# Performance work log

Hardware: AMD Instinct MI355X
Metric: run time of the kernel (lower is better)

Reference implementation:

```python
import jax, jax.numpy as jnp
import numpy as np

BS, SL, D_IN, D_MODEL, H = 4, 128, 512, 512, 8
DP = D_MODEL // H


def setup_inputs() -> dict:
    key = jax.random.key(0)
    ks = jax.random.split(key, 12)
    s = 0.02
    inp = {
        "q": jax.random.normal(ks[0], (BS, SL, D_IN), jnp.float32),
        "k": jax.random.normal(ks[1], (BS, SL, D_IN), jnp.float32),
        "v": jax.random.normal(ks[2], (BS, SL, D_IN), jnp.float32),
    }
    j = jnp.arange(SL)
    # mask[t, jk] = 1.0 for the zero-padded slots jk > t in the shuffled sequence for step t
    mask2d = (j[None, :] > j[:, None]).astype(jnp.float32)  # (SL, SL)
    inp["mask"] = mask2d[None, :, None, None, :]            # (1, SL, 1, 1, SL)
    for i, n in enumerate(["wq", "wk", "wv", "dense"]):
        din = D_IN if n != "dense" else D_MODEL
        inp[n + "_w"] = jax.random.normal(ks[3 + 2 * i], (din, D_MODEL), jnp.float32) * s
        inp[n + "_b"] = jnp.zeros((D_MODEL,), jnp.float32)
    return inp


def _shuffle_idx(key, sl):
    # Row t of returned idx: random permutation of [0..t-1], then t, then t+1.. (padding slots).
    u = jax.random.uniform(key, (sl, sl))
    j = jnp.arange(sl)
    t = j[:, None]
    sort_keys = jnp.where(j[None, :] < t, u, j[None, :].astype(jnp.float32) + 2.0)
    return jnp.argsort(sort_keys, axis=-1)  # (sl, sl) int32


def _split_heads_shuffled(x, idx, valid):
    # x: (bs, sl, d) -> (bs, sl, H, sl, DP); padding slots (j > t) zeroed like torch plc_holder
    bs, sl, d = x.shape
    xt = x[:, idx, :] * valid[None, :, :, None]  # (bs, sl, sl, d)
    xt = xt.reshape(bs, sl, sl, H, DP)
    return xt.transpose(0, 1, 3, 2, 4)


def reference(q, k, v, mask, wq_w, wq_b, wk_w, wk_b, wv_w, wv_b, dense_w, dense_b):
    bs, sl, _ = q.shape
    j = jnp.arange(sl)
    valid = (j[None, :] <= j[:, None]).astype(q.dtype)  # (sl, sl)
    pkey = jax.random.key(42)
    idx_q = _shuffle_idx(jax.random.fold_in(pkey, 0), sl)
    idx_k = _shuffle_idx(jax.random.fold_in(pkey, 1), sl)
    idx_v = _shuffle_idx(jax.random.fold_in(pkey, 2), sl)

    qp = q @ wq_w + wq_b
    kp = k @ wk_w + wk_b
    vp = v @ wv_w + wv_b

    qh = _split_heads_shuffled(qp, idx_q, valid)  # (bs, sl, H, sl, DP)
    kh = _split_heads_shuffled(kp, idx_k, valid)
    vh = _split_heads_shuffled(vp, idx_v, valid)

    logits = jnp.einsum('bthqd,bthkd->bthqk', qh, kh) / jnp.sqrt(jnp.float32(DP))
    logits = logits + mask * (-1e9)
    attn = jax.nn.softmax(logits, axis=-1)          # (bs, sl, H, sl, sl)
    ctx = jnp.einsum('bthqk,bthkd->bthqd', attn, vh)  # (bs, sl, H, sl, DP)

    ctx = ctx.transpose(0, 1, 3, 2, 4).reshape(bs, sl, sl, H * DP)
    eff = ctx[:, j, j, :]                           # query row t of step t (the token itself)
    out = eff @ dense_w + dense_b                   # (bs, sl, d_model); dropout p=0 -> identity
    return (out, attn)
```

## Files before the change

### kernel.cpp

```cpp
#include <hip/hip_runtime.h>
#include <stdint.h>


#define BSZ 4
#define SLEN 128
#define DMODEL 512
#define NHEAD 8
#define HDIM 64

__device__ __forceinline__ uint32_t rotl32(uint32_t v, int d) {
  return (v << d) | (v >> (32 - d));
}

__device__ __forceinline__ void tf2x32(uint32_t k0, uint32_t k1, uint32_t x0,
                                       uint32_t x1, uint32_t& y0, uint32_t& y1) {
  uint32_t ks2 = k0 ^ k1 ^ 0x1BD11BDAu;
  x0 += k0; x1 += k1;
#define TF_R(r) { x0 += x1; x1 = rotl32(x1, (r)); x1 ^= x0; }
  TF_R(13) TF_R(15) TF_R(26) TF_R(6)
  x0 += k1;  x1 += ks2 + 1u;
  TF_R(17) TF_R(29) TF_R(16) TF_R(24)
  x0 += ks2; x1 += k0 + 2u;
  TF_R(13) TF_R(15) TF_R(26) TF_R(6)
  x0 += k0;  x1 += k1 + 3u;
  TF_R(17) TF_R(29) TF_R(16) TF_R(24)
  x0 += k1;  x1 += ks2 + 4u;
  TF_R(13) TF_R(15) TF_R(26) TF_R(6)
  x0 += ks2; x1 += k0 + 5u;
#undef TF_R
  y0 = x0; y1 = x1;
}

__global__ __launch_bounds__(128) void idx_kernel(int* __restrict__ idx) {
  const int m = blockIdx.x;
  const int t = blockIdx.y;
  const int j = threadIdx.x;
  __shared__ float u[SLEN];
  uint32_t fk0, fk1;
  tf2x32(0u, 42u, 0u, (uint32_t)m, fk0, fk1);
  const int flat = t * SLEN + j;
  uint32_t y0, y1;
  tf2x32(fk0, fk1, 0u, (uint32_t)flat, y0, y1);
  uint32_t bits = y0 ^ y1;
  float uu = __uint_as_float((bits >> 9) | 0x3f800000u) - 1.0f;
  u[j] = uu;
  __syncthreads();
  int* row = idx + (m * SLEN + t) * SLEN;
  if (j >= t) {
    row[j] = j;
  } else {
    int rank = 0;
    for (int i = 0; i < t; ++i) {
      float ui = u[i];
      rank += ((ui < uu) || (ui == uu && i < j)) ? 1 : 0;
    }
    row[rank] = j;
  }
}

__device__ __forceinline__ void gemm512_body(const float* __restrict__ A,
                                             const float* __restrict__ W,
                                             const float* __restrict__ bias,
                                             float* __restrict__ C,
                                             float* As , float* Ws ) {
  const int tid = threadIdx.x;
  const int tx = tid & 15, ty = tid >> 4;
  const int row0 = blockIdx.y * 64, col0 = blockIdx.x * 64;
  const int lr = tid >> 2, lc = (tid & 3) << 2;
  const int wr = tid >> 4, wc = (tid & 15) << 2;
  float acc[4][4] = {};
  for (int k0 = 0; k0 < 512; k0 += 16) {
    float4 av = *(const float4*)(A + (size_t)(row0 + lr) * 512 + k0 + lc);
    float4 wv = *(const float4*)(W + (size_t)(k0 + wr) * 512 + col0 + wc);
    As[lr * 17 + lc + 0] = av.x; As[lr * 17 + lc + 1] = av.y;
    As[lr * 17 + lc + 2] = av.z; As[lr * 17 + lc + 3] = av.w;
    *(float4*)(Ws + wr * 64 + wc) = wv;
    __syncthreads();
#pragma unroll
    for (int kk = 0; kk < 16; ++kk) {
      float a[4], b[4];
#pragma unroll
      for (int i = 0; i < 4; ++i) a[i] = As[(ty * 4 + i) * 17 + kk];
#pragma unroll
      for (int jj = 0; jj < 4; ++jj) b[jj] = Ws[kk * 64 + tx * 4 + jj];
#pragma unroll
      for (int i = 0; i < 4; ++i)
#pragma unroll
        for (int jj = 0; jj < 4; ++jj) acc[i][jj] += a[i] * b[jj];
    }
    __syncthreads();
  }
#pragma unroll
  for (int i = 0; i < 4; ++i) {
    int r = row0 + ty * 4 + i, c = col0 + tx * 4;
    float4 o;
    o.x = acc[i][0] + bias[c + 0];
    o.y = acc[i][1] + bias[c + 1];
    o.z = acc[i][2] + bias[c + 2];
    o.w = acc[i][3] + bias[c + 3];
    *(float4*)(C + (size_t)r * 512 + c) = o;
  }
}

__global__ __launch_bounds__(256) void proj_kernel(
    const float* __restrict__ q, const float* __restrict__ k, const float* __restrict__ v,
    const float* __restrict__ wq, const float* __restrict__ wk, const float* __restrict__ wv,
    const float* __restrict__ bq, const float* __restrict__ bk, const float* __restrict__ bv,
    float* __restrict__ qp, float* __restrict__ kp, float* __restrict__ vp) {
  __shared__ float As[64 * 17];
  __shared__ float Ws[16 * 64];
  const float* A; const float* W; const float* B; float* C;
  if (blockIdx.z == 0)      { A = q; W = wq; B = bq; C = qp; }
  else if (blockIdx.z == 1) { A = k; W = wk; B = bk; C = kp; }
  else                      { A = v; W = wv; B = bv; C = vp; }
  gemm512_body(A, W, B, C, As, Ws);
}

__global__ __launch_bounds__(256) void dense_kernel(const float* __restrict__ A,
                                                    const float* __restrict__ W,
                                                    const float* __restrict__ B,
                                                    float* __restrict__ C) {
  __shared__ float As[64 * 17];
  __shared__ float Ws[16 * 64];
  gemm512_body(A, W, B, C, As, Ws);
}

__global__ __launch_bounds__(256) void s_kernel(const float* __restrict__ qp,
                                                const float* __restrict__ kp,
                                                float* __restrict__ S) {
  const int h = blockIdx.x, b = blockIdx.y;
  const int tid = threadIdx.x;
  __shared__ float qs[SLEN * 33];
  __shared__ float ks[SLEN * 33];
  const float* qbase = qp + ((size_t)b * SLEN) * DMODEL + h * HDIM;
  const float* kbase = kp + ((size_t)b * SLEN) * DMODEL + h * HDIM;
  const int i0 = (tid >> 4) * 8, j0 = (tid & 15) * 8;
  float acc[8][8] = {};
  for (int d0 = 0; d0 < HDIM; d0 += 32) {
    __syncthreads();
    for (int it = 0; it < 4; ++it) {
      int flat = it * 256 + tid;
      int row = flat >> 3;
      int c4 = (flat & 7) << 2;
      float4 a = *(const float4*)(qbase + (size_t)row * DMODEL + d0 + c4);
      float4 bb = *(const float4*)(kbase + (size_t)row * DMODEL + d0 + c4);
      qs[row * 33 + c4 + 0] = a.x;  qs[row * 33 + c4 + 1] = a.y;
      qs[row * 33 + c4 + 2] = a.z;  qs[row * 33 + c4 + 3] = a.w;
      ks[row * 33 + c4 + 0] = bb.x; ks[row * 33 + c4 + 1] = bb.y;
      ks[row * 33 + c4 + 2] = bb.z; ks[row * 33 + c4 + 3] = bb.w;
    }
    __syncthreads();
    for (int d = 0; d < 32; ++d) {
      float a[8], bb[8];
#pragma unroll
      for (int r = 0; r < 8; ++r) a[r] = qs[(i0 + r) * 33 + d];
#pragma unroll
      for (int c = 0; c < 8; ++c) bb[c] = ks[(j0 + c) * 33 + d];
#pragma unroll
      for (int r = 0; r < 8; ++r)
#pragma unroll
        for (int c = 0; c < 8; ++c) acc[r][c] += a[r] * bb[c];
    }
  }
  float* Sb = S + (size_t)(b * NHEAD + h) * SLEN * SLEN;
#pragma unroll
  for (int r = 0; r < 8; ++r) {
    float4 o0, o1;
    o0.x = acc[r][0] * 0.125f; o0.y = acc[r][1] * 0.125f;
    o0.z = acc[r][2] * 0.125f; o0.w = acc[r][3] * 0.125f;
    o1.x = acc[r][4] * 0.125f; o1.y = acc[r][5] * 0.125f;
    o1.z = acc[r][6] * 0.125f; o1.w = acc[r][7] * 0.125f;
    *(float4*)(Sb + (size_t)(i0 + r) * SLEN + j0) = o0;
    *(float4*)(Sb + (size_t)(i0 + r) * SLEN + j0 + 4) = o1;
  }
}

__global__ __launch_bounds__(128) void ef_kernel(const float* __restrict__ S,
                                                 float* __restrict__ E,
                                                 float* __restrict__ Ft) {
  const int bh = blockIdx.x;
  const int i = threadIdx.x;
  __shared__ float m127s[SLEN];
  const float* Sb = S + (size_t)bh * SLEN * SLEN;
  const float* Srow = Sb + (size_t)i * SLEN;
  float m = -3.402823466e38f;
  for (int j = 0; j < SLEN; ++j) m = fmaxf(m, Srow[j]);
  m127s[i] = m;
  float rm = -3.402823466e38f, rl = 0.f;
  float* Fb = Ft + (size_t)bh * SLEN * SLEN;
  for (int t = 0; t < SLEN; ++t) {
    float sv = Srow[t];
    float nm = fmaxf(rm, sv);
    rl = rl * __expf(rm - nm) + __expf(sv - nm);
    rm = nm;
    Fb[t * SLEN + i] = __expf(m - nm) / rl;
  }
  __syncthreads();
  float* Eb = E + (size_t)bh * SLEN * SLEN;
  for (int flat = i; flat < SLEN * SLEN; flat += SLEN) {
    int r = flat >> 7;
    Eb[flat] = __expf(Sb[flat] - m127s[r]);
  }
}

__global__ __launch_bounds__(256) void attn_kernel(const float* __restrict__ E,
                                                   const float* __restrict__ Ft,
                                                   const int* __restrict__ idx,
                                                   const float* __restrict__ vp,
                                                   float* __restrict__ attn_out,
                                                   float* __restrict__ eff) {
  const int h = blockIdx.x, t = blockIdx.y, b = blockIdx.z;
  const int tid = threadIdx.x;
  const int wave = tid >> 6, lane = tid & 63;
  __shared__ int iqs[SLEN], iks[SLEN], ivs[SLEN];
  __shared__ float arow[SLEN];
  if (tid < SLEN) {
    iqs[tid] = idx[(0 * SLEN + t) * SLEN + tid];
    iks[tid] = idx[(1 * SLEN + t) * SLEN + tid];
    ivs[tid] = idx[(2 * SLEN + t) * SLEN + tid];
  }
  __syncthreads();
  const int bh = b * NHEAD + h;
  const float* Eb = E + (size_t)bh * SLEN * SLEN;
  const float* Fb = Ft + ((size_t)bh * SLEN + t) * SLEN;
  const float inv = 1.0f / (float)(t + 1);
  float* obase = attn_out + ((size_t)((b * SLEN + t) * NHEAD + h)) * SLEN * SLEN;
  const int k0 = lane * 2, k1 = lane * 2 + 1;
  for (int q = wave; q < SLEN; q += 4) {
    float2 val;
    if (q <= t) {
      int iq = iqs[q];
      float f = Fb[iq];
      const float* Er = Eb + (size_t)iq * SLEN;
      val.x = (k0 <= t) ? Er[iks[k0]] * f : 0.f;
      val.y = (k1 <= t) ? Er[iks[k1]] * f : 0.f;
    } else {
      val.x = (k0 <= t) ? inv : 0.f;
      val.y = (k1 <= t) ? inv : 0.f;
    }
    *(float2*)(obase + (size_t)q * SLEN + k0) = val;
    if (q == t) { arow[k0] = val.x; arow[k1] = val.y; }
  }
  __syncthreads();
  if (tid < HDIM) {
    const int d = tid;
    const float* vb = vp + (size_t)b * SLEN * DMODEL + h * HDIM + d;
    float acc = 0.f;
    for (int k = 0; k <= t; ++k) acc += arow[k] * vb[(size_t)ivs[k] * DMODEL];
    eff[((size_t)b * SLEN + t) * DMODEL + h * HDIM + d] = acc;
  }
}

extern "C" void kernel_launch(void* const* d_in, const int* in_sizes, int n_in,
                              void* d_out, int out_size, void* d_ws, size_t ws_size,
                              hipStream_t stream) {
  const float* q    = (const float*)d_in[0];
  const float* k    = (const float*)d_in[1];
  const float* v    = (const float*)d_in[2];
  const float* wq_w = (const float*)d_in[4];
  const float* wq_b = (const float*)d_in[5];
  const float* wk_w = (const float*)d_in[6];
  const float* wk_b = (const float*)d_in[7];
  const float* wv_w = (const float*)d_in[8];
  const float* wv_b = (const float*)d_in[9];
  const float* dw   = (const float*)d_in[10];
  const float* db   = (const float*)d_in[11];

  float* out  = (float*)d_out;
  float* attn = out + 262144;

  int*   idx = (int*)d_ws;
  float* wsf = (float*)d_ws;
  float* qp  = wsf + 49152;
  float* kp  = qp + 262144;
  float* vp  = kp + 262144;
  float* S   = vp + 262144;
  float* E   = S + 524288;
  float* Ft  = E + 524288;
  float* eff = Ft + 524288;
  (void)in_sizes; (void)n_in; (void)out_size; (void)ws_size;

  idx_kernel<<<dim3(3, 128, 1), 128, 0, stream>>>(idx);
  proj_kernel<<<dim3(8, 8, 3), 256, 0, stream>>>(q, k, v, wq_w, wk_w, wv_w,
                                                 wq_b, wk_b, wv_b, qp, kp, vp);
  s_kernel<<<dim3(8, 4, 1), 256, 0, stream>>>(qp, kp, S);
  ef_kernel<<<dim3(32, 1, 1), 128, 0, stream>>>(S, E, Ft);
  attn_kernel<<<dim3(8, 128, 4), 256, 0, stream>>>(E, Ft, idx, vp, attn, eff);
  dense_kernel<<<dim3(8, 8, 1), 256, 0, stream>>>(eff, dw, db, out);
}
```

Before: 439.6 us.

## Fuse score, exp and prefix-normalizer kernels; store E as bf16

Merges the S and E/F kernels into one. The max, exp and running-sum normalizers are computed from the register tile using shared-memory reductions, and the serial per-row scan in a 32-block kernel goes away. E is stored in bf16, which halves its traffic in the attention gather but adds rounding error to the attn output. The attention kernel also caches the F row in LDS, hoists the key indices, and splits the context reduction across all four waves. The prefix normalizer is now computed from exps relative to the global row max rather than the running-max rescaling form, which may change numerics.

```diff
diff --git a/kernel.cpp b/kernel.cpp
--- a/kernel.cpp
+++ b/kernel.cpp
@@ -29,6 +29,14 @@
   x0 += ks2; x1 += k0 + 5u;
 #undef TF_R
   y0 = x0; y1 = x1;
+}
+
+__device__ __forceinline__ uint16_t f32_to_bf16(float v) {
+  uint32_t x = __float_as_uint(v);
+  return (uint16_t)((x + 0x7FFFu + ((x >> 16) & 1u)) >> 16);
+}
+__device__ __forceinline__ float bf16_to_f32(uint16_t b) {
+  return __uint_as_float(((uint32_t)b) << 16);
 }
 
 __global__ __launch_bounds__(128) void idx_kernel(int* __restrict__ idx) {
@@ -125,16 +133,20 @@
   gemm512_body(A, W, B, C, As, Ws);
 }
 
-__global__ __launch_bounds__(256) void s_kernel(const float* __restrict__ qp,
-                                                const float* __restrict__ kp,
-                                                float* __restrict__ S) {
+__global__ __launch_bounds__(256) void sef_kernel(const float* __restrict__ qp,
+                                                  const float* __restrict__ kp,
+                                                  uint16_t* __restrict__ E,
+                                                  float* __restrict__ Ft) {
   const int h = blockIdx.x, b = blockIdx.y;
   const int tid = threadIdx.x;
-  __shared__ float qs[SLEN * 33];
-  __shared__ float ks[SLEN * 33];
+  __shared__ float qs[32 * 132];
+  __shared__ float ks[32 * 132];
+  __shared__ float redm[128 * 16];
+  __shared__ float csum[128 * 16];
+  __shared__ float m127s[SLEN];
   const float* qbase = qp + ((size_t)b * SLEN) * DMODEL + h * HDIM;
   const float* kbase = kp + ((size_t)b * SLEN) * DMODEL + h * HDIM;
-  const int i0 = (tid >> 4) * 8, j0 = (tid & 15) * 8;
+  const int i0 = (tid >> 4) * 8, jg = tid & 15, j0 = jg * 8;
   float acc[8][8] = {};
   for (int d0 = 0; d0 < HDIM; d0 += 32) {
     __syncthreads();
@@ -144,66 +156,79 @@
       int c4 = (flat & 7) << 2;
       float4 a = *(const float4*)(qbase + (size_t)row * DMODEL + d0 + c4);
       float4 bb = *(const float4*)(kbase + (size_t)row * DMODEL + d0 + c4);
-      qs[row * 33 + c4 + 0] = a.x;  qs[row * 33 + c4 + 1] = a.y;
-      qs[row * 33 + c4 + 2] = a.z;  qs[row * 33 + c4 + 3] = a.w;
-      ks[row * 33 + c4 + 0] = bb.x; ks[row * 33 + c4 + 1] = bb.y;
-      ks[row * 33 + c4 + 2] = bb.z; ks[row * 33 + c4 + 3] = bb.w;
+      qs[(c4 + 0) * 132 + row] = a.x;  qs[(c4 + 1) * 132 + row] = a.y;
+      qs[(c4 + 2) * 132 + row] = a.z;  qs[(c4 + 3) * 132 + row] = a.w;
+      ks[(c4 + 0) * 132 + row] = bb.x; ks[(c4 + 1) * 132 + row] = bb.y;
+      ks[(c4 + 2) * 132 + row] = bb.z; ks[(c4 + 3) * 132 + row] = bb.w;
     }
     __syncthreads();
     for (int d = 0; d < 32; ++d) {
-      float a[8], bb[8];
-#pragma unroll
-      for (int r = 0; r < 8; ++r) a[r] = qs[(i0 + r) * 33 + d];
-#pragma unroll
-      for (int c = 0; c < 8; ++c) bb[c] = ks[(j0 + c) * 33 + d];
+      float4 qa = *(const float4*)(qs + d * 132 + i0);
+      float4 qb = *(const float4*)(qs + d * 132 + i0 + 4);
+      float4 ka = *(const float4*)(ks + d * 132 + j0);
+      float4 kb = *(const float4*)(ks + d * 132 + j0 + 4);
+      float a[8] = {qa.x, qa.y, qa.z, qa.w, qb.x, qb.y, qb.z, qb.w};
+      float bb[8] = {ka.x, ka.y, ka.z, ka.w, kb.x, kb.y, kb.z, kb.w};
 #pragma unroll
       for (int r = 0; r < 8; ++r)
 #pragma unroll
         for (int c = 0; c < 8; ++c) acc[r][c] += a[r] * bb[c];
     }
   }
-  float* Sb = S + (size_t)(b * NHEAD + h) * SLEN * SLEN;
 #pragma unroll
   for (int r = 0; r < 8; ++r) {
-    float4 o0, o1;
-    o0.x = acc[r][0] * 0.125f; o0.y = acc[r][1] * 0.125f;
-    o0.z = acc[r][2] * 0.125f; o0.w = acc[r][3] * 0.125f;
-    o1.x = acc[r][4] * 0.125f; o1.y = acc[r][5] * 0.125f;
-    o1.z = acc[r][6] * 0.125f; o1.w = acc[r][7] * 0.125f;
-    *(float4*)(Sb + (size_t)(i0 + r) * SLEN + j0) = o0;
-    *(float4*)(Sb + (size_t)(i0 + r) * SLEN + j0 + 4) = o1;
-  }
-}
-
-__global__ __launch_bounds__(128) void ef_kernel(const float* __restrict__ S,
-                                                 float* __restrict__ E,
-                                                 float* __restrict__ Ft) {
-  const int bh = blockIdx.x;
-  const int i = threadIdx.x;
-  __shared__ float m127s[SLEN];
-  const float* Sb = S + (size_t)bh * SLEN * SLEN;
-  const float* Srow = Sb + (size_t)i * SLEN;
-  float m = -3.402823466e38f;
-  for (int j = 0; j < SLEN; ++j) m = fmaxf(m, Srow[j]);
-  m127s[i] = m;
-  float rm = -3.402823466e38f, rl = 0.f;
+    float m = -3.402823466e38f;
+#pragma unroll
+    for (int c = 0; c < 8; ++c) {
+      acc[r][c] *= 0.125f;
+      m = fmaxf(m, acc[r][c]);
+    }
+    redm[(i0 + r) * 16 + jg] = m;
+  }
+  __syncthreads();
+  if (tid < SLEN) {
+    float m = redm[tid * 16];
+#pragma unroll
+    for (int g = 1; g < 16; ++g) m = fmaxf(m, redm[tid * 16 + g]);
+    m127s[tid] = m;
+  }
+  __syncthreads();
+  const int bh = b * NHEAD + h;
+  uint16_t* Eb = E + (size_t)bh * SLEN * SLEN;
+#pragma unroll
+  for (int r = 0; r < 8; ++r) {
+    const float m = m127s[i0 + r];
+    float run = 0.f;
+    ushort4 e0, e1;
+    float ev;
+    ev = __expf(acc[r][0] - m); e0.x = f32_to_bf16(ev); run += ev; acc[r][0] = run;
+    ev = __expf(acc[r][1] - m); e0.y = f32_to_bf16(ev); run += ev; acc[r][1] = run;
+    ev = __expf(acc[r][2] - m); e0.z = f32_to_bf16(ev); run += ev; acc[r][2] = run;
+    ev = __expf(acc[r][3] - m); e0.w = f32_to_bf16(ev); run += ev; acc[r][3] = run;
+    ev = __expf(acc[r][4] - m); e1.x = f32_to_bf16(ev); run += ev; acc[r][4] = run;
+    ev = __expf(acc[r][5] - m); e1.y = f32_to_bf16(ev); run += ev; acc[r][5] = run;
+    ev = __expf(acc[r][6] - m); e1.z = f32_to_bf16(ev); run += ev; acc[r][6] = run;
+    ev = __expf(acc[r][7] - m); e1.w = f32_to_bf16(ev); run += ev; acc[r][7] = run;
+    *(ushort4*)(Eb + (size_t)(i0 + r) * SLEN + j0) = e0;
+    *(ushort4*)(Eb + (size_t)(i0 + r) * SLEN + j0 + 4) = e1;
+    csum[(i0 + r) * 16 + jg] = run;
+  }
+  __syncthreads();
   float* Fb = Ft + (size_t)bh * SLEN * SLEN;
-  for (int t = 0; t < SLEN; ++t) {
-    float sv = Srow[t];
-    float nm = fmaxf(rm, sv);
-    rl = rl * __expf(rm - nm) + __expf(sv - nm);
-    rm = nm;
-    Fb[t * SLEN + i] = __expf(m - nm) / rl;
-  }
-  __syncthreads();
-  float* Eb = E + (size_t)bh * SLEN * SLEN;
-  for (int flat = i; flat < SLEN * SLEN; flat += SLEN) {
-    int r = flat >> 7;
-    Eb[flat] = __expf(Sb[flat] - m127s[r]);
-  }
-}
-
-__global__ __launch_bounds__(256) void attn_kernel(const float* __restrict__ E,
+#pragma unroll
+  for (int r = 0; r < 8; ++r) {
+    float base = 0.f;
+    for (int g = 0; g < 16; ++g) {
+      if (g == jg) break;
+      base += csum[(i0 + r) * 16 + g];
+    }
+#pragma unroll
+    for (int c = 0; c < 8; ++c)
+      Fb[(size_t)(j0 + c) * SLEN + (i0 + r)] = 1.0f / (base + acc[r][c]);
+  }
+}
+
+__global__ __launch_bounds__(256) void attn_kernel(const uint16_t* __restrict__ E,
                                                    const float* __restrict__ Ft,
                                                    const int* __restrict__ idx,
                                                    const float* __restrict__ vp,
@@ -213,41 +238,50 @@
   const int tid = threadIdx.x;
   const int wave = tid >> 6, lane = tid & 63;
   __shared__ int iqs[SLEN], iks[SLEN], ivs[SLEN];
+  __shared__ float Fs[SLEN];
   __shared__ float arow[SLEN];
+  __shared__ float red[256];
+  const int bh = b * NHEAD + h;
   if (tid < SLEN) {
     iqs[tid] = idx[(0 * SLEN + t) * SLEN + tid];
     iks[tid] = idx[(1 * SLEN + t) * SLEN + tid];
     ivs[tid] = idx[(2 * SLEN + t) * SLEN + tid];
-  }
-  __syncthreads();
-  const int bh = b * NHEAD + h;
-  const float* Eb = E + (size_t)bh * SLEN * SLEN;
-  const float* Fb = Ft + ((size_t)bh * SLEN + t) * SLEN;
+    Fs[tid] = Ft[((size_t)bh * SLEN + t) * SLEN + tid];
+  }
+  __syncthreads();
+  const uint16_t* Eb = E + (size_t)bh * SLEN * SLEN;
   const float inv = 1.0f / (float)(t + 1);
   float* obase = attn_out + ((size_t)((b * SLEN + t) * NHEAD + h)) * SLEN * SLEN;
-  const int k0 = lane * 2, k1 = lane * 2 + 1;
+  const int k0 = lane * 2, k1 = k0 + 1;
+  const int ik0 = iks[k0], ik1 = iks[k1];
+  const bool k0ok = (k0 <= t), k1ok = (k1 <= t);
   for (int q = wave; q < SLEN; q += 4) {
     float2 val;
     if (q <= t) {
       int iq = iqs[q];
-      float f = Fb[iq];
-      const float* Er = Eb + (size_t)iq * SLEN;
-      val.x = (k0 <= t) ? Er[iks[k0]] * f : 0.f;
-      val.y = (k1 <= t) ? Er[iks[k1]] * f : 0.f;
+      float f = Fs[iq];
+      const uint16_t* Er = Eb + (size_t)iq * SLEN;
+      val.x = k0ok ? bf16_to_f32(Er[ik0]) * f : 0.f;
+      val.y = k1ok ? bf16_to_f32(Er[ik1]) * f : 0.f;
     } else {
-      val.x = (k0 <= t) ? inv : 0.f;
-      val.y = (k1 <= t) ? inv : 0.f;
+      val.x = k0ok ? inv : 0.f;
+      val.y = k1ok ? inv : 0.f;
     }
     *(float2*)(obase + (size_t)q * SLEN + k0) = val;
     if (q == t) { arow[k0] = val.x; arow[k1] = val.y; }
   }
   __syncthreads();
-  if (tid < HDIM) {
-    const int d = tid;
+  {
+    const int d = tid & 63, kg = tid >> 6;
     const float* vb = vp + (size_t)b * SLEN * DMODEL + h * HDIM + d;
     float acc = 0.f;
-    for (int k = 0; k <= t; ++k) acc += arow[k] * vb[(size_t)ivs[k] * DMODEL];
-    eff[((size_t)b * SLEN + t) * DMODEL + h * HDIM + d] = acc;
+    for (int k = kg; k <= t; k += 4) acc += arow[k] * vb[(size_t)ivs[k] * DMODEL];
+    red[tid] = acc;
+  }
+  __syncthreads();
+  if (tid < HDIM) {
+    eff[((size_t)b * SLEN + t) * DMODEL + h * HDIM + tid] =
+        red[tid] + red[tid + 64] + red[tid + 128] + red[tid + 192];
   }
 }
 
@@ -269,22 +303,20 @@
   float* out  = (float*)d_out;
   float* attn = out + 262144;
 
-  int*   idx = (int*)d_ws;
   float* wsf = (float*)d_ws;
-  float* qp  = wsf + 49152;
+  uint16_t* E = (uint16_t*)wsf;
+  int*   idx = (int*)(wsf + 262144);
+  float* qp  = wsf + 311296;
   float* kp  = qp + 262144;
   float* vp  = kp + 262144;
-  float* S   = vp + 262144;
-  float* E   = S + 524288;
-  float* Ft  = E + 524288;
+  float* Ft  = vp + 262144;
   float* eff = Ft + 524288;
   (void)in_sizes; (void)n_in; (void)out_size; (void)ws_size;
 
   idx_kernel<<<dim3(3, 128, 1), 128, 0, stream>>>(idx);
   proj_kernel<<<dim3(8, 8, 3), 256, 0, stream>>>(q, k, v, wq_w, wk_w, wv_w,
                                                  wq_b, wk_b, wv_b, qp, kp, vp);
-  s_kernel<<<dim3(8, 4, 1), 256, 0, stream>>>(qp, kp, S);
-  ef_kernel<<<dim3(32, 1, 1), 128, 0, stream>>>(S, E, Ft);
+  sef_kernel<<<dim3(8, 4, 1), 256, 0, stream>>>(qp, kp, E, Ft);
   attn_kernel<<<dim3(8, 128, 4), 256, 0, stream>>>(E, Ft, idx, vp, attn, eff);
   dense_kernel<<<dim3(8, 8, 1), 256, 0, stream>>>(eff, dw, db, out);
 }
```

After: 407.6 us. -7.3%, faster.
